# Kernel optimization log

Hardware: AMD Instinct MI355X
Metric: run time of the kernel (lower is better)

Reference implementation:

```python
import jax, jax.numpy as jnp
import numpy as np

N, F_IN, F_OUT = 8192, 256, 128


def setup_inputs() -> dict:
    key = jax.random.key(0)
    k1, k2, k3, k4 = jax.random.split(key, 4)
    h = jax.random.normal(k1, (N, F_IN), dtype=jnp.float32)
    adj = jax.random.randint(k2, (N, N), 0, 2, dtype=jnp.int32)
    # xavier-uniform-like init scales
    w_lim = float(np.sqrt(6.0 / (F_IN + F_OUT)))
    a_lim = float(np.sqrt(6.0 / (2 * F_OUT + 1)))
    W = jax.random.uniform(k3, (F_IN, F_OUT), jnp.float32, -w_lim, w_lim)
    a = jax.random.uniform(k4, (2 * F_OUT, 1), jnp.float32, -a_lim, a_lim)
    return {"h": h, "adj": adj, "W": W, "a": a}


def reference(h, adj, W, a):
    # Wh: [N, F_OUT]
    Wh = h @ W
    # Fused form of the pairwise-concat score: e[i,j] = leakyrelu(Wh_i.a1 + Wh_j.a2)
    a1 = a[:F_OUT]   # [F_OUT, 1]
    a2 = a[F_OUT:]   # [F_OUT, 1]
    s1 = Wh @ a1     # [N, 1]
    s2 = Wh @ a2     # [N, 1]
    e = jax.nn.leaky_relu(s1 + s2.T, negative_slope=0.2)  # [N, N]
    e = jnp.where(adj > 0, e, jnp.float32(-9e15))
    attention = jax.nn.softmax(e, axis=1)
    return attention @ Wh  # [N, F_OUT]
```

## Files before the change

### kernel.cpp

```cpp
#include <hip/hip_runtime.h>

#define N_   8192
#define FIN  256
#define FOUT 128

typedef _Float16 f16x8 __attribute__((ext_vector_type(8)));
typedef float    f32x4 __attribute__((ext_vector_type(4)));
typedef unsigned int uint;

__global__ __launch_bounds__(256) void k_wh(
    const float* __restrict__ h, const float* __restrict__ W,
    const float* __restrict__ a, float* __restrict__ Wh,
    float* __restrict__ s1, float* __restrict__ s2)
{
    __shared__ float hrow[2][FIN];
    __shared__ float rbuf[2][2][2];
    const int t   = threadIdx.x;
    const int rh  = t >> 7;
    const int c   = t & 127;
    const int row = (blockIdx.x << 1) + rh;

    hrow[rh][c]       = h[(size_t)row * FIN + c];
    hrow[rh][c + 128] = h[(size_t)row * FIN + c + 128];
    __syncthreads();

    float acc = 0.f;
    #pragma unroll 8
    for (int k = 0; k < FIN; ++k)
        acc = fmaf(hrow[rh][k], W[k * FOUT + c], acc);

    Wh[(size_t)row * FOUT + c] = acc;

    float p1 = acc * a[c];
    float p2 = acc * a[FOUT + c];
    #pragma unroll
    for (int off = 32; off; off >>= 1) {
        p1 += __shfl_down(p1, off, 64);
        p2 += __shfl_down(p2, off, 64);
    }
    if ((t & 63) == 0) { rbuf[rh][c >> 6][0] = p1; rbuf[rh][c >> 6][1] = p2; }
    __syncthreads();
    if (c == 0) {
        const float k2 = 1.44269504088896f;
        s1[row] = (rbuf[rh][0][0] + rbuf[rh][1][0]) * k2;
        s2[row] = (rbuf[rh][0][1] + rbuf[rh][1][1]) * k2;
    }
}

__global__ __launch_bounds__(256) void k_tr(
    const float* __restrict__ Wh, _Float16* __restrict__ WhTt)
{
    __shared__ float tile[64][129];
    const int t = threadIdx.x;
    const int rbase = blockIdx.x * 64;

    #pragma unroll
    for (int q = 0; q < 8; ++q) {
        int i4 = q * 256 + t;
        int r  = i4 >> 5;
        int c4 = (i4 & 31) * 4;
        *(float4*)&tile[r][c4] = *(const float4*)&Wh[(size_t)(rbase + r) * FOUT + c4];
    }
    __syncthreads();

    const int c = t >> 1, half = t & 1;
    _Float16 buf[32];
    #pragma unroll
    for (int r = 0; r < 32; ++r) buf[r] = (_Float16)tile[32 * half + r][c];
    _Float16* dst = WhTt + (size_t)(rbase / 32 + half) * 4096 + c * 32;
    #pragma unroll
    for (int q = 0; q < 4; ++q)
        *(f16x8*)(dst + 8 * q) = *(f16x8*)&buf[8 * q];
}

__global__ __launch_bounds__(256) void k_attn(
    const int* __restrict__ adj, const _Float16* __restrict__ WhTt,
    const float* __restrict__ s1g, const float* __restrict__ s2g,
    float* __restrict__ num_g, float* __restrict__ den_g)
{
    const int t  = threadIdx.x;
    const int w  = t >> 6;
    const int l  = t & 63;
    const int ln15 = l & 15, lq = l >> 4;

    const int sp    = blockIdx.x >> 7;
    const int rg    = (blockIdx.x & 127) * 4 + w;
    const int rbase = rg * 16;
    const int jbase = sp * 2048;

    const float s1r = s1g[rbase + ln15];
    const int* __restrict__ arow =
        adj + (size_t)(rbase + ln15) * N_ + jbase + 8 * lq;
    const float* __restrict__ s2p = s2g + jbase + 8 * lq;
    const _Float16* __restrict__ bp =
        WhTt + (size_t)(jbase >> 5) * 4096 + ln15 * 32 + 8 * lq;

    f32x4 acc[8];
    #pragma unroll
    for (int g = 0; g < 8; ++g) acc[g] = (f32x4){0.f, 0.f, 0.f, 0.f};
    float denp = 0.f;

    auto LA = [&](int tile, int h) { return *(const int4*)(arow + tile * 32 + 4 * h); };
    auto LS = [&](int tile, int h) { return *(const float4*)(s2p + tile * 32 + 4 * h); };

    auto loadB = [&](f16x8* Bd, int tile) {
        const _Float16* p = bp + (size_t)tile * 4096;
        #pragma unroll
        for (int g = 0; g < 8; ++g) Bd[g] = *(const f16x8*)(p + g * 512);
    };

    auto computeP = [&](const int4& a0, const int4& a1,
                        const float4& sA, const float4& sB) -> f16x8 {
        const float bias = -5.77078016f;
        float m, e;
        f16x8 pv;
        m = s1r + sA.x; e = fmaxf(m, 0.2f * m); pv[0] = (_Float16)(a0.x ? __builtin_amdgcn_exp2f(e + bias) : 0.f);
        m = s1r + sA.y; e = fmaxf(m, 0.2f * m); pv[1] = (_Float16)(a0.y ? __builtin_amdgcn_exp2f(e + bias) : 0.f);
        m = s1r + sA.z; e = fmaxf(m, 0.2f * m); pv[2] = (_Float16)(a0.z ? __builtin_amdgcn_exp2f(e + bias) : 0.f);
        m = s1r + sA.w; e = fmaxf(m, 0.2f * m); pv[3] = (_Float16)(a0.w ? __builtin_amdgcn_exp2f(e + bias) : 0.f);
        m = s1r + sB.x; e = fmaxf(m, 0.2f * m); pv[4] = (_Float16)(a1.x ? __builtin_amdgcn_exp2f(e + bias) : 0.f);
        m = s1r + sB.y; e = fmaxf(m, 0.2f * m); pv[5] = (_Float16)(a1.y ? __builtin_amdgcn_exp2f(e + bias) : 0.f);
        m = s1r + sB.z; e = fmaxf(m, 0.2f * m); pv[6] = (_Float16)(a1.z ? __builtin_amdgcn_exp2f(e + bias) : 0.f);
        m = s1r + sB.w; e = fmaxf(m, 0.2f * m); pv[7] = (_Float16)(a1.w ? __builtin_amdgcn_exp2f(e + bias) : 0.f);
        denp += (float)pv[0] + (float)pv[1] + (float)pv[2] + (float)pv[3]
              + (float)pv[4] + (float)pv[5] + (float)pv[6] + (float)pv[7];
        return pv;
    };

    auto mmaAll = [&](const f16x8& af, const f16x8* B) {
        __builtin_amdgcn_s_setprio(1);
        #pragma unroll
        for (int g = 0; g < 8; ++g)
            acc[g] = __builtin_amdgcn_mfma_f32_16x16x32_f16(af, B[g], acc[g], 0, 0, 0);
        __builtin_amdgcn_s_setprio(0);
    };

    int4   aA0 = LA(0, 0), aA1 = LA(0, 1);
    int4   aB0 = LA(1, 0), aB1 = LA(1, 1);
    float4 sA0 = LS(0, 0), sA1 = LS(0, 1);
    float4 sB0, sB1;
    f16x8  Bc[8], Bn[8];
    loadB(Bc, 0);

    for (int tt = 0; tt < 64; tt += 2) {
        {
            const int tn = (tt + 1 < 64) ? tt + 1 : 63;
            sB0 = LS(tn, 0); sB1 = LS(tn, 1);
            loadB(Bn, tn);
            f16x8 af = computeP(aA0, aA1, sA0, sA1);
            const int ta = (tt + 2 < 64) ? tt + 2 : 63;
            aA0 = LA(ta, 0); aA1 = LA(ta, 1);
            mmaAll(af, Bc);
        }
        {
            const int tn = (tt + 2 < 64) ? tt + 2 : 63;
            sA0 = LS(tn, 0); sA1 = LS(tn, 1);
            loadB(Bc, tn);
            f16x8 af = computeP(aB0, aB1, sB0, sB1);
            const int ta = (tt + 3 < 64) ? tt + 3 : 63;
            aB0 = LA(ta, 0); aB1 = LA(ta, 1);
            mmaAll(af, Bn);
        }
    }

    denp += __shfl_xor(denp, 16, 64);
    denp += __shfl_xor(denp, 32, 64);
    if (l < 16)
        den_g[(size_t)sp * N_ + rbase + ln15] = denp;

    #pragma unroll
    for (int g = 0; g < 8; ++g) {
        #pragma unroll
        for (int e = 0; e < 4; ++e)
            num_g[((size_t)sp * N_ + rbase + 4 * lq + e) * FOUT + 16 * g + ln15] = acc[g][e];
    }
}

__global__ __launch_bounds__(256) void k_norm(
    const float* __restrict__ num_g, const float* __restrict__ den_g,
    float* __restrict__ out)
{
    const int idx4 = blockIdx.x * 256 + threadIdx.x;
    const int i  = idx4 >> 5;
    const int c4 = (idx4 & 31) * 4;

    float4 s = {0.f, 0.f, 0.f, 0.f};
    float  d = 0.f;
    #pragma unroll
    for (int sp = 0; sp < 4; ++sp) {
        float4 v = *(const float4*)(num_g + ((size_t)sp * N_ + i) * FOUT + c4);
        s.x += v.x; s.y += v.y; s.z += v.z; s.w += v.w;
        d += den_g[(size_t)sp * N_ + i];
    }
    const float inv = 1.f / d;
    float4 o = {s.x * inv, s.y * inv, s.z * inv, s.w * inv};
    *(float4*)&out[(size_t)i * FOUT + c4] = o;
}

extern "C" void kernel_launch(void* const* d_in, const int* in_sizes, int n_in,
                              void* d_out, int out_size, void* d_ws, size_t ws_size,
                              hipStream_t stream) {
    const float* h   = (const float*)d_in[0];
    const int*   adj = (const int*)d_in[1];
    const float* W   = (const float*)d_in[2];
    const float* a   = (const float*)d_in[3];
    float* out = (float*)d_out;

    char* ws = (char*)d_ws;
    float*    Wh   = (float*)ws;
    _Float16* WhTt = (_Float16*)(ws + (4u << 20));
    float*    s1   = (float*)(ws + (6u << 20));
    float*    s2   = (float*)(ws + (6u << 20) + 32768);
    float*    num  = (float*)(ws + (7u << 20));
    float*    den  = (float*)(ws + (23u << 20));

    k_wh  <<<N_ / 2, 256, 0, stream>>>(h, W, a, Wh, s1, s2);
    k_tr  <<<N_ / 64, 256, 0, stream>>>(Wh, WhTt);
    k_attn<<<512,   256, 0, stream>>>(adj, WhTt, s1, s2, num, den);
    k_norm<<<1024,  256, 0, stream>>>(num, den, out);
}
```

Measured before the change: 163.5 us.

## Pack adjacency into bitmask, split attention 8-way, store partial numerators in fp16

Adds a pre-pass that packs the int32 adjacency matrix into a per-row bitmask, and the attention kernel now reads mask bits instead of full int4 vectors. The adjacency matrix is still read once in full by the pack kernel, so the gain depends on the attention kernel having been latency-bound on its interleaved adjacency loads. The column split grows from 4 to 8 partitions (1024 blocks) to raise parallelism. Partial numerators are stored as fp16 to halve the reduction traffic, which adds rounding error and one extra kernel launch.

```diff
diff --git a/kernel.cpp b/kernel.cpp
--- a/kernel.cpp
+++ b/kernel.cpp
@@ -3,10 +3,33 @@
 #define N_   8192
 #define FIN  256
 #define FOUT 128
+#define NW   (N_ / 32)
 
 typedef _Float16 f16x8 __attribute__((ext_vector_type(8)));
+typedef _Float16 f16x4 __attribute__((ext_vector_type(4)));
 typedef float    f32x4 __attribute__((ext_vector_type(4)));
 typedef unsigned int uint;
+
+__global__ __launch_bounds__(256) void k_pack(
+    const int* __restrict__ adj, uint* __restrict__ bm)
+{
+    const int wid = (blockIdx.x * 256 + threadIdx.x) >> 6;
+    const int l   = threadIdx.x & 63;
+    const int4* __restrict__ arow = (const int4*)(adj + (size_t)wid * N_);
+    uint* __restrict__ brow = bm + (size_t)wid * NW;
+
+    #pragma unroll 2
+    for (int jb = 0; jb < 32; ++jb) {
+        int4 av = arow[jb * 64 + l];
+        uint nib = (uint)(av.x != 0) | ((uint)(av.y != 0) << 1)
+                 | ((uint)(av.z != 0) << 2) | ((uint)(av.w != 0) << 3);
+        uint v = nib | (__shfl_xor(nib, 1, 64) << 4);
+        v = v | (__shfl_xor(v, 2, 64) << 8);
+        v = v | (__shfl_xor(v, 4, 64) << 16);
+        if ((l & 7) == 0)
+            brow[jb * 8 + (l >> 3)] = v;
+    }
+}
 
 __global__ __launch_bounds__(256) void k_wh(
     const float* __restrict__ h, const float* __restrict__ W,
@@ -74,110 +97,106 @@
 }
 
 __global__ __launch_bounds__(256) void k_attn(
-    const int* __restrict__ adj, const _Float16* __restrict__ WhTt,
+    const uint* __restrict__ bm, const _Float16* __restrict__ WhTt,
     const float* __restrict__ s1g, const float* __restrict__ s2g,
-    float* __restrict__ num_g, float* __restrict__ den_g)
-{
-    const int t  = threadIdx.x;
-    const int w  = t >> 6;
-    const int l  = t & 63;
+    _Float16* __restrict__ num_g, float* __restrict__ den_g)
+{
+    const int t = threadIdx.x;
+    const int w = t >> 6, l = t & 63;
     const int ln15 = l & 15, lq = l >> 4;
-
-    const int sp    = blockIdx.x >> 7;
-    const int rg    = (blockIdx.x & 127) * 4 + w;
-    const int rbase = rg * 16;
-    const int jbase = sp * 2048;
-
-    const float s1r = s1g[rbase + ln15];
-    const int* __restrict__ arow =
-        adj + (size_t)(rbase + ln15) * N_ + jbase + 8 * lq;
-    const float* __restrict__ s2p = s2g + jbase + 8 * lq;
-    const _Float16* __restrict__ bp =
-        WhTt + (size_t)(jbase >> 5) * 4096 + ln15 * 32 + 8 * lq;
+    const int shiftM = lq << 3;
+
+    const int sp    = blockIdx.x & 7;
+    const int rblk  = blockIdx.x >> 3;
+    const int rbase = rblk * 64 + w * 16;
+    const int jbase = sp * 1024;
+
+    const int   row = rbase + ln15;
+    const float s1r = s1g[row];
+    const uint*     __restrict__ mrow = bm + (size_t)row * NW + sp * 32;
+    const float*    __restrict__ s2p  = s2g + jbase + 8 * lq;
+    const _Float16* __restrict__ bp   =
+        WhTt + (size_t)(sp * 32) * 4096 + ln15 * 32 + 8 * lq;
 
     f32x4 acc[8];
     #pragma unroll
     for (int g = 0; g < 8; ++g) acc[g] = (f32x4){0.f, 0.f, 0.f, 0.f};
     float denp = 0.f;
 
-    auto LA = [&](int tile, int h) { return *(const int4*)(arow + tile * 32 + 4 * h); };
-    auto LS = [&](int tile, int h) { return *(const float4*)(s2p + tile * 32 + 4 * h); };
-
-    auto loadB = [&](f16x8* Bd, int tile) {
-        const _Float16* p = bp + (size_t)tile * 4096;
-        #pragma unroll
-        for (int g = 0; g < 8; ++g) Bd[g] = *(const f16x8*)(p + g * 512);
-    };
-
-    auto computeP = [&](const int4& a0, const int4& a1,
-                        const float4& sA, const float4& sB) -> f16x8 {
+    auto sub = [&](int tt, uint& mk, const float4& sa0, const float4& sa1,
+                   float4& sb0, float4& sb1) {
+        const _Float16* bt = bp + (size_t)tt * 4096;
+        f16x8 B0 = *(const f16x8*)(bt);
+        f16x8 B1 = *(const f16x8*)(bt + 512);
+        f16x8 B2 = *(const f16x8*)(bt + 1024);
+        f16x8 B3 = *(const f16x8*)(bt + 1536);
+        f16x8 B4 = *(const f16x8*)(bt + 2048);
+        f16x8 B5 = *(const f16x8*)(bt + 2560);
+        f16x8 B6 = *(const f16x8*)(bt + 3072);
+        f16x8 B7 = *(const f16x8*)(bt + 3584);
+
+        const int tn = (tt + 1 < 32) ? tt + 1 : 31;
+        sb0 = *(const float4*)(s2p + tn * 32);
+        sb1 = *(const float4*)(s2p + tn * 32 + 4);
+
         const float bias = -5.77078016f;
+        const uint byte = (mk >> shiftM) & 255u;
         float m, e;
         f16x8 pv;
-        m = s1r + sA.x; e = fmaxf(m, 0.2f * m); pv[0] = (_Float16)(a0.x ? __builtin_amdgcn_exp2f(e + bias) : 0.f);
-        m = s1r + sA.y; e = fmaxf(m, 0.2f * m); pv[1] = (_Float16)(a0.y ? __builtin_amdgcn_exp2f(e + bias) : 0.f);
-        m = s1r + sA.z; e = fmaxf(m, 0.2f * m); pv[2] = (_Float16)(a0.z ? __builtin_amdgcn_exp2f(e + bias) : 0.f);
-        m = s1r + sA.w; e = fmaxf(m, 0.2f * m); pv[3] = (_Float16)(a0.w ? __builtin_amdgcn_exp2f(e + bias) : 0.f);
-        m = s1r + sB.x; e = fmaxf(m, 0.2f * m); pv[4] = (_Float16)(a1.x ? __builtin_amdgcn_exp2f(e + bias) : 0.f);
-        m = s1r + sB.y; e = fmaxf(m, 0.2f * m); pv[5] = (_Float16)(a1.y ? __builtin_amdgcn_exp2f(e + bias) : 0.f);
-        m = s1r + sB.z; e = fmaxf(m, 0.2f * m); pv[6] = (_Float16)(a1.z ? __builtin_amdgcn_exp2f(e + bias) : 0.f);
-        m = s1r + sB.w; e = fmaxf(m, 0.2f * m); pv[7] = (_Float16)(a1.w ? __builtin_amdgcn_exp2f(e + bias) : 0.f);
+        m = s1r + sa0.x; e = fmaxf(m, 0.2f * m); pv[0] = (_Float16)((byte & 1u)   ? __builtin_amdgcn_exp2f(e + bias) : 0.f);
+        m = s1r + sa0.y; e = fmaxf(m, 0.2f * m); pv[1] = (_Float16)((byte & 2u)   ? __builtin_amdgcn_exp2f(e + bias) : 0.f);
+        m = s1r + sa0.z; e = fmaxf(m, 0.2f * m); pv[2] = (_Float16)((byte & 4u)   ? __builtin_amdgcn_exp2f(e + bias) : 0.f);
+        m = s1r + sa0.w; e = fmaxf(m, 0.2f * m); pv[3] = (_Float16)((byte & 8u)   ? __builtin_amdgcn_exp2f(e + bias) : 0.f);
+        m = s1r + sa1.x; e = fmaxf(m, 0.2f * m); pv[4] = (_Float16)((byte & 16u)  ? __builtin_amdgcn_exp2f(e + bias) : 0.f);
+        m = s1r + sa1.y; e = fmaxf(m, 0.2f * m); pv[5] = (_Float16)((byte & 32u)  ? __builtin_amdgcn_exp2f(e + bias) : 0.f);
+        m = s1r + sa1.z; e = fmaxf(m, 0.2f * m); pv[6] = (_Float16)((byte & 64u)  ? __builtin_amdgcn_exp2f(e + bias) : 0.f);
+        m = s1r + sa1.w; e = fmaxf(m, 0.2f * m); pv[7] = (_Float16)((byte & 128u) ? __builtin_amdgcn_exp2f(e + bias) : 0.f);
         denp += (float)pv[0] + (float)pv[1] + (float)pv[2] + (float)pv[3]
               + (float)pv[4] + (float)pv[5] + (float)pv[6] + (float)pv[7];
-        return pv;
-    };
-
-    auto mmaAll = [&](const f16x8& af, const f16x8* B) {
+
+        const int ta = (tt + 4 < 32) ? tt + 4 : 31;
+        mk = mrow[ta];
+
         __builtin_amdgcn_s_setprio(1);
-        #pragma unroll
-        for (int g = 0; g < 8; ++g)
-            acc[g] = __builtin_amdgcn_mfma_f32_16x16x32_f16(af, B[g], acc[g], 0, 0, 0);
+        acc[0] = __builtin_amdgcn_mfma_f32_16x16x32_f16(pv, B0, acc[0], 0, 0, 0);
+        acc[1] = __builtin_amdgcn_mfma_f32_16x16x32_f16(pv, B1, acc[1], 0, 0, 0);
+        acc[2] = __builtin_amdgcn_mfma_f32_16x16x32_f16(pv, B2, acc[2], 0, 0, 0);
+        acc[3] = __builtin_amdgcn_mfma_f32_16x16x32_f16(pv, B3, acc[3], 0, 0, 0);
+        acc[4] = __builtin_amdgcn_mfma_f32_16x16x32_f16(pv, B4, acc[4], 0, 0, 0);
+        acc[5] = __builtin_amdgcn_mfma_f32_16x16x32_f16(pv, B5, acc[5], 0, 0, 0);
+        acc[6] = __builtin_amdgcn_mfma_f32_16x16x32_f16(pv, B6, acc[6], 0, 0, 0);
+        acc[7] = __builtin_amdgcn_mfma_f32_16x16x32_f16(pv, B7, acc[7], 0, 0, 0);
         __builtin_amdgcn_s_setprio(0);
     };
 
-    int4   aA0 = LA(0, 0), aA1 = LA(0, 1);
-    int4   aB0 = LA(1, 0), aB1 = LA(1, 1);
-    float4 sA0 = LS(0, 0), sA1 = LS(0, 1);
+    uint mk0 = mrow[0], mk1 = mrow[1], mk2 = mrow[2], mk3 = mrow[3];
+    float4 sA0 = *(const float4*)(s2p);
+    float4 sA1 = *(const float4*)(s2p + 4);
     float4 sB0, sB1;
-    f16x8  Bc[8], Bn[8];
-    loadB(Bc, 0);
-
-    for (int tt = 0; tt < 64; tt += 2) {
-        {
-            const int tn = (tt + 1 < 64) ? tt + 1 : 63;
-            sB0 = LS(tn, 0); sB1 = LS(tn, 1);
-            loadB(Bn, tn);
-            f16x8 af = computeP(aA0, aA1, sA0, sA1);
-            const int ta = (tt + 2 < 64) ? tt + 2 : 63;
-            aA0 = LA(ta, 0); aA1 = LA(ta, 1);
-            mmaAll(af, Bc);
-        }
-        {
-            const int tn = (tt + 2 < 64) ? tt + 2 : 63;
-            sA0 = LS(tn, 0); sA1 = LS(tn, 1);
-            loadB(Bc, tn);
-            f16x8 af = computeP(aB0, aB1, sB0, sB1);
-            const int ta = (tt + 3 < 64) ? tt + 3 : 63;
-            aB0 = LA(ta, 0); aB1 = LA(ta, 1);
-            mmaAll(af, Bn);
-        }
+
+    for (int tt = 0; tt < 32; tt += 4) {
+        sub(tt,     mk0, sA0, sA1, sB0, sB1);
+        sub(tt + 1, mk1, sB0, sB1, sA0, sA1);
+        sub(tt + 2, mk2, sA0, sA1, sB0, sB1);
+        sub(tt + 3, mk3, sB0, sB1, sA0, sA1);
     }
 
     denp += __shfl_xor(denp, 16, 64);
     denp += __shfl_xor(denp, 32, 64);
     if (l < 16)
-        den_g[(size_t)sp * N_ + rbase + ln15] = denp;
+        den_g[(size_t)sp * N_ + row] = denp;
 
     #pragma unroll
     for (int g = 0; g < 8; ++g) {
         #pragma unroll
         for (int e = 0; e < 4; ++e)
-            num_g[((size_t)sp * N_ + rbase + 4 * lq + e) * FOUT + 16 * g + ln15] = acc[g][e];
+            num_g[((size_t)sp * N_ + rbase + 4 * lq + e) * FOUT + 16 * g + ln15]
+                = (_Float16)acc[g][e];
     }
 }
 
 __global__ __launch_bounds__(256) void k_norm(
-    const float* __restrict__ num_g, const float* __restrict__ den_g,
+    const _Float16* __restrict__ num_g, const float* __restrict__ den_g,
     float* __restrict__ out)
 {
     const int idx4 = blockIdx.x * 256 + threadIdx.x;
@@ -187,9 +206,10 @@
     float4 s = {0.f, 0.f, 0.f, 0.f};
     float  d = 0.f;
     #pragma unroll
-    for (int sp = 0; sp < 4; ++sp) {
-        float4 v = *(const float4*)(num_g + ((size_t)sp * N_ + i) * FOUT + c4);
-        s.x += v.x; s.y += v.y; s.z += v.z; s.w += v.w;
+    for (int sp = 0; sp < 8; ++sp) {
+        f16x4 v = *(const f16x4*)(num_g + ((size_t)sp * N_ + i) * FOUT + c4);
+        s.x += (float)v[0]; s.y += (float)v[1];
+        s.z += (float)v[2]; s.w += (float)v[3];
         d += den_g[(size_t)sp * N_ + i];
     }
     const float inv = 1.f / d;
@@ -211,11 +231,13 @@
     _Float16* WhTt = (_Float16*)(ws + (4u << 20));
     float*    s1   = (float*)(ws + (6u << 20));
     float*    s2   = (float*)(ws + (6u << 20) + 32768);
-    float*    num  = (float*)(ws + (7u << 20));
+    _Float16* num  = (_Float16*)(ws + (7u << 20));
     float*    den  = (float*)(ws + (23u << 20));
-
+    uint*     bmk  = (uint*)(ws + (24u << 20));
+
+    k_pack<<<2048,   256, 0, stream>>>(adj, bmk);
     k_wh  <<<N_ / 2, 256, 0, stream>>>(h, W, a, Wh, s1, s2);
     k_tr  <<<N_ / 64, 256, 0, stream>>>(Wh, WhTt);
-    k_attn<<<512,   256, 0, stream>>>(adj, WhTt, s1, s2, num, den);
+    k_attn<<<1024,  256, 0, stream>>>(bmk, WhTt, s1, s2, num, den);
     k_norm<<<1024,  256, 0, stream>>>(num, den, out);
 }
```

Result: slower. 181.9 us (+11.3%).
